# Kernel tuning notes

Hardware: AMD Instinct MI355X
Metric: run time of the kernel (lower is better)

The kernel has to match this reference:

```python
import jax, jax.numpy as jnp
import numpy as np

N_NODES = 100000
N_EDGES = 1600000
D_IN = 128
D_OUT = 128


def setup_inputs() -> dict:
    key = jax.random.key(0)
    k1, k2, k3, k4, k5 = jax.random.split(key, 5)
    x = jax.random.normal(k1, (N_NODES, D_IN), dtype=jnp.float32)
    # nn.Linear weight has shape [out_features, in_features]
    W = jax.random.normal(k2, (D_OUT, D_IN), dtype=jnp.float32) * (1.0 / np.sqrt(D_IN))
    adj_rows = jax.random.randint(k3, (N_EDGES,), 0, N_NODES, dtype=jnp.int32)
    adj_cols = jax.random.randint(k4, (N_EDGES,), 0, N_NODES, dtype=jnp.int32)
    adj_vals = jax.random.uniform(k5, (N_EDGES,), dtype=jnp.float32)
    return {"x": x, "W": W, "adj_rows": adj_rows, "adj_cols": adj_cols, "adj_vals": adj_vals}


def reference(x, W, adj_rows, adj_cols, adj_vals):
    # x: [N, D_in] node features; W: [D_out, D_in] linear weight (bias=False)
    h = jnp.einsum('ni,oi->no', x, W)  # dense projection, [N, D_out]
    # sparse adjacency matmul: out[r] = sum_e vals[e] * h[cols[e]] for rows[e]==r
    messages = adj_vals[:, None] * h[adj_cols]  # [E, D_out]
    out = jax.ops.segment_sum(messages, adj_rows, num_segments=x.shape[0])
    return out
```

## Files before the change

kernel.cpp:

```cpp
#include <hip/hip_runtime.h>

#define D 128
#define RPB 512
#define RPB_SHIFT 9
#define HALF 256
#define BUCKMAX 256
#define TILE 8192
#define SEGCAP 7168

typedef short bf16x8 __attribute__((ext_vector_type(8)));
typedef float f32x4 __attribute__((ext_vector_type(4)));

__device__ inline unsigned short f2bf(float f) {
    unsigned u = __float_as_uint(f);
    unsigned r = u + 0x7FFFu + ((u >> 16) & 1u);
    return (unsigned short)(r >> 16);
}

__global__ __launch_bounds__(256) void cast_bf16(const float* __restrict__ src,
                                                 unsigned short* __restrict__ dst,
                                                 long long n4) {
    long long i = (long long)blockIdx.x * 256 + threadIdx.x;
    const long long stride = (long long)gridDim.x * 256;
    for (; i < n4; i += stride) {
        float4 v = reinterpret_cast<const float4*>(src)[i];
        ushort4 o;
        o.x = f2bf(v.x); o.y = f2bf(v.y); o.z = f2bf(v.z); o.w = f2bf(v.w);
        reinterpret_cast<ushort4*>(dst)[i] = o;
    }
}

__global__ __launch_bounds__(1024) void bucket_hist(const int* __restrict__ rows,
                                                    int* __restrict__ bucketCnt,
                                                    int E, int NBUCK) {
    __shared__ int h[BUCKMAX];
    for (int i = threadIdx.x; i < NBUCK; i += 1024) h[i] = 0;
    __syncthreads();
    const int t0 = blockIdx.x * TILE;
    const int tend = min(t0 + TILE, E);
    for (int i = t0 + threadIdx.x; i < tend; i += 1024)
        atomicAdd(&h[rows[i] >> RPB_SHIFT], 1);
    __syncthreads();
    for (int i = threadIdx.x; i < NBUCK; i += 1024)
        if (h[i]) atomicAdd(&bucketCnt[i], h[i]);
}

__global__ __launch_bounds__(256) void bucket_scan(const int* __restrict__ bucketCnt,
                                                   int* __restrict__ bucketBase,
                                                   int* __restrict__ bucketCur,
                                                   int* __restrict__ offsets,
                                                   int NBUCK, int N) {
    __shared__ int t[256];
    const int tid = threadIdx.x;
    int v = (tid < NBUCK) ? bucketCnt[tid] : 0;
    t[tid] = v;
    __syncthreads();
    for (int ofs = 1; ofs < 256; ofs <<= 1) {
        int add = (tid >= ofs) ? t[tid - ofs] : 0;
        __syncthreads();
        t[tid] += add;
        __syncthreads();
    }
    if (tid < NBUCK) {
        bucketBase[tid] = t[tid] - v;
        bucketCur[tid] = 0;
    }
    if (tid == NBUCK - 1) {
        bucketBase[NBUCK] = t[tid];
        offsets[N] = t[tid];
    }
}

__global__ __launch_bounds__(1024) void binA(const int* __restrict__ rows,
                                             const int* __restrict__ cols,
                                             const float* __restrict__ vals,
                                             const int* __restrict__ bucketBase,
                                             int* __restrict__ bucketCur,
                                             uint2* __restrict__ pairs_bin,
                                             int E, int NBUCK) {
    __shared__ int h[BUCKMAX];
    __shared__ int base[BUCKMAX];
    const int t0 = blockIdx.x * TILE;
    const int tend = min(t0 + TILE, E);
    for (int i = threadIdx.x; i < NBUCK; i += 1024) h[i] = 0;
    __syncthreads();
    for (int i = t0 + threadIdx.x; i < tend; i += 1024)
        atomicAdd(&h[rows[i] >> RPB_SHIFT], 1);
    __syncthreads();
    for (int i = threadIdx.x; i < NBUCK; i += 1024) {
        int c = h[i];
        base[i] = c ? bucketBase[i] + atomicAdd(&bucketCur[i], c) : 0;
        h[i] = 0;
    }
    __syncthreads();
    for (int i = t0 + threadIdx.x; i < tend; i += 1024) {
        int r = rows[i];
        int b = r >> RPB_SHIFT;
        int p = base[b] + atomicAdd(&h[b], 1);
        unsigned pk = ((unsigned)(r & (RPB - 1)) << 23) | (unsigned)cols[i];
        pairs_bin[p] = make_uint2(pk, __float_as_uint(vals[i]));
    }
}

__global__ __launch_bounds__(256) void csr_build(const uint2* __restrict__ pairs_bin,
                                                 const int* __restrict__ bucketBase,
                                                 int* __restrict__ offsets,
                                                 uint2* __restrict__ pairs_g, int N) {
    __shared__ int hist[HALF];
    __shared__ int cur[HALF];
    __shared__ int tsum[256];
    __shared__ uint2 pr[SEGCAP];
    __shared__ int cntBelowSh;
    const int tid = threadIdx.x;
    const int buck = blockIdx.x >> 1, half = blockIdx.x & 1;
    const int lrow0 = half * HALF;
    const int grow0 = buck * RPB + lrow0;
    const int rbeg = bucketBase[buck], rend = bucketBase[buck + 1];

    hist[tid] = 0;
    if (tid == 0) cntBelowSh = 0;
    __syncthreads();

    int below = 0;
    for (int i = rbeg + tid; i < rend; i += 256) {
        int d = (int)(pairs_bin[i].x >> 23) - lrow0;
        if ((unsigned)d < (unsigned)HALF) atomicAdd(&hist[d], 1);
        else if (d < 0) ++below;
    }
    if (below) atomicAdd(&cntBelowSh, below);
    __syncthreads();

    int part = hist[tid];
    tsum[tid] = part;
    __syncthreads();
    for (int ofs = 1; ofs < 256; ofs <<= 1) {
        int add = (tid >= ofs) ? tsum[tid - ofs] : 0;
        __syncthreads();
        tsum[tid] += add;
        __syncthreads();
    }
    const int excl = tsum[tid] - part;
    const int segcnt = tsum[255];
    const int segbase = rbeg + cntBelowSh;

    cur[tid] = excl;
    const int grow = grow0 + tid;
    if (grow < N) offsets[grow] = segbase + excl;
    __syncthreads();

    if (segcnt <= SEGCAP) {
        for (int i = rbeg + tid; i < rend; i += 256) {
            uint2 e = pairs_bin[i];
            int d = (int)(e.x >> 23) - lrow0;
            if ((unsigned)d < (unsigned)HALF) {
                int p = atomicAdd(&cur[d], 1);
                pr[p] = make_uint2(e.x & 0x7FFFFFu, e.y);
            }
        }
        __syncthreads();
        for (int p = tid; p < segcnt; p += 256) pairs_g[segbase + p] = pr[p];
    } else {
        for (int i = rbeg + tid; i < rend; i += 256) {
            uint2 e = pairs_bin[i];
            int d = (int)(e.x >> 23) - lrow0;
            if ((unsigned)d < (unsigned)HALF) {
                int p = atomicAdd(&cur[d], 1);
                pairs_g[segbase + p] = make_uint2(e.x & 0x7FFFFFu, e.y);
            }
        }
    }
}

__global__ __launch_bounds__(256) void csr_gather_bf16(
    const unsigned short* __restrict__ xb,
    const int* __restrict__ offsets,
    const uint2* __restrict__ pairs,
    unsigned short* __restrict__ yb, int N) {
    const int row = blockIdx.x * 4 + (threadIdx.x >> 6);
    if (row >= N) return;
    const int lane = threadIdx.x & 63;
    const int beg = offsets[row], end = offsets[row + 1];
    float ax = 0.f, ay = 0.f;

    for (int base = beg; base < end; base += 64) {
        const int rem = min(end - base, 64);
        uint2 e = make_uint2(0u, 0u);
        if (lane < rem) e = pairs[base + lane];
        int c = (int)e.x;
        float v = __uint_as_float(e.y);

        for (int j0 = 0; j0 < rem; j0 += 8) {
            int cj[8];
            float vj[8];
            unsigned u[8];
#pragma unroll
            for (int jj = 0; jj < 8; ++jj) {
                cj[jj] = __shfl(c, j0 + jj);
                vj[jj] = __shfl(v, j0 + jj);
            }
#pragma unroll
            for (int jj = 0; jj < 8; ++jj)
                u[jj] = *reinterpret_cast<const unsigned*>(
                    xb + (size_t)cj[jj] * D + lane * 2);
#pragma unroll
            for (int jj = 0; jj < 8; ++jj) {
                ax = fmaf(vj[jj], __uint_as_float(u[jj] << 16), ax);
                ay = fmaf(vj[jj], __uint_as_float(u[jj] & 0xFFFF0000u), ay);
            }
        }
    }
    unsigned o = (unsigned)f2bf(ax) | ((unsigned)f2bf(ay) << 16);
    *reinterpret_cast<unsigned*>(yb + (size_t)row * D + lane * 2) = o;
}

__global__ __launch_bounds__(256) void gemm_mfma(const unsigned short* __restrict__ yb,
                                                 const unsigned short* __restrict__ Wb,
                                                 float* __restrict__ out, int N) {
    const int wid  = threadIdx.x >> 6;
    const int lane = threadIdx.x & 63;
    const int m0   = blockIdx.x * 64 + wid * 16;
    const int r    = lane & 15;
    const int kg   = lane >> 4;
    const int arow = m0 + r;

    f32x4 acc[8] = {};
#pragma unroll
    for (int ks = 0; ks < 4; ++ks) {
        const int k0 = ks * 32 + kg * 8;
        bf16x8 a = {};
        if (arow < N) a = *reinterpret_cast<const bf16x8*>(yb + (size_t)arow * D + k0);
#pragma unroll
        for (int t = 0; t < 8; ++t) {
            bf16x8 b = *reinterpret_cast<const bf16x8*>(Wb + (size_t)(t * 16 + r) * D + k0);
            acc[t] = __builtin_amdgcn_mfma_f32_16x16x32_bf16(a, b, acc[t], 0, 0, 0);
        }
    }
#pragma unroll
    for (int t = 0; t < 8; ++t) {
#pragma unroll
        for (int i = 0; i < 4; ++i) {
            const int row = m0 + kg * 4 + i;
            if (row < N) out[(size_t)row * D + t * 16 + r] = acc[t][i];
        }
    }
}

__global__ __launch_bounds__(256) void gemm64(const float* __restrict__ x,
                                              const float* __restrict__ W,
                                              float* __restrict__ h, int N) {
    __shared__ float xs[128][64];
    __shared__ float ws[128][64];
    const int tid = threadIdx.x;
    const int m0 = blockIdx.x * 64;
    const int n0 = blockIdx.y * 64;
    for (int idx = tid; idx < 2048; idx += 256) {
        int q = idx >> 6, m = idx & 63;
        int grow = m0 + m;
        float4 v = make_float4(0.f, 0.f, 0.f, 0.f);
        if (grow < N) v = *reinterpret_cast<const float4*>(x + (size_t)grow * D + q * 4);
        xs[q * 4 + 0][m] = v.x; xs[q * 4 + 1][m] = v.y;
        xs[q * 4 + 2][m] = v.z; xs[q * 4 + 3][m] = v.w;
    }
    for (int idx = tid; idx < 2048; idx += 256) {
        int q = idx >> 6, n = idx & 63;
        float4 v = *reinterpret_cast<const float4*>(W + (size_t)(n0 + n) * D + q * 4);
        ws[q * 4 + 0][n] = v.x; ws[q * 4 + 1][n] = v.y;
        ws[q * 4 + 2][n] = v.z; ws[q * 4 + 3][n] = v.w;
    }
    __syncthreads();
    const int tm = (tid & 15) * 4;
    const int tn = (tid >> 4) * 4;
    float acc[4][4] = {};
#pragma unroll 4
    for (int k = 0; k < 128; ++k) {
        float4 a4 = *reinterpret_cast<const float4*>(&xs[k][tm]);
        float4 b4 = *reinterpret_cast<const float4*>(&ws[k][tn]);
        float a[4] = {a4.x, a4.y, a4.z, a4.w};
        float b[4] = {b4.x, b4.y, b4.z, b4.w};
#pragma unroll
        for (int rr = 0; rr < 4; ++rr)
#pragma unroll
            for (int cc = 0; cc < 4; ++cc) acc[rr][cc] = fmaf(a[rr], b[cc], acc[rr][cc]);
    }
#pragma unroll
    for (int rr = 0; rr < 4; ++rr) {
        int row = m0 + tm + rr;
        if (row < N) {
            float4 o = make_float4(acc[rr][0], acc[rr][1], acc[rr][2], acc[rr][3]);
            *reinterpret_cast<float4*>(h + (size_t)row * D + n0 + tn) = o;
        }
    }
}

__global__ __launch_bounds__(256) void scatter_edges(const float* __restrict__ h,
                                                     const int* __restrict__ rows,
                                                     const int* __restrict__ cols,
                                                     const float* __restrict__ vals,
                                                     float* __restrict__ out, int E) {
    int t = blockIdx.x * 256 + threadIdx.x;
    int e = t >> 5;
    if (e >= E) return;
    int q = t & 31;
    int r = rows[e];
    int c = cols[e];
    float v = vals[e];
    float4 m = reinterpret_cast<const float4*>(h + (size_t)c * D)[q];
    float* op = out + (size_t)r * D + q * 4;
    atomicAdd(op + 0, v * m.x);
    atomicAdd(op + 1, v * m.y);
    atomicAdd(op + 2, v * m.z);
    atomicAdd(op + 3, v * m.w);
}

extern "C" void kernel_launch(void* const* d_in, const int* in_sizes, int n_in,
                              void* d_out, int out_size, void* d_ws, size_t ws_size,
                              hipStream_t stream) {
    const float* x        = (const float*)d_in[0];
    const float* W        = (const float*)d_in[1];
    const int*   adj_rows = (const int*)d_in[2];
    const int*   adj_cols = (const int*)d_in[3];
    const float* adj_vals = (const float*)d_in[4];
    float* out = (float*)d_out;

    const int N = in_sizes[0] / D;
    const int E = in_sizes[2];
    const int NBUCK = (N + RPB - 1) / RPB;
    const int NT = (E + TILE - 1) / TILE;

    size_t off = 0;
    auto carve = [&](size_t bytes) {
        void* p = (char*)d_ws + off;
        off += (bytes + 255) & ~(size_t)255;
        return p;
    };
    unsigned short* xb = (unsigned short*)carve((size_t)N * D * 2);
    unsigned short* yb = (unsigned short*)carve((size_t)N * D * 2);
    unsigned short* Wb = (unsigned short*)carve((size_t)D * D * 2);
    int* offsets    = (int*)carve((size_t)(N + 1) * sizeof(int));
    int* bucketCnt  = (int*)carve((size_t)BUCKMAX * sizeof(int));
    int* bucketBase = (int*)carve((size_t)(BUCKMAX + 1) * sizeof(int));
    int* bucketCur  = (int*)carve((size_t)BUCKMAX * sizeof(int));
    const size_t wsNeed = off;

    size_t doff = 0;
    auto carveOut = [&](size_t bytes) {
        void* p = (char*)d_out + doff;
        doff += (bytes + 255) & ~(size_t)255;
        return p;
    };
    uint2* pairs_bin = (uint2*)carveOut((size_t)E * sizeof(uint2));
    uint2* pairs_g   = (uint2*)carveOut((size_t)E * sizeof(uint2));
    const size_t doutNeed = doff;

    const bool fits = (wsNeed <= ws_size) &&
                      (doutNeed <= (size_t)out_size * sizeof(float)) &&
                      (NBUCK <= BUCKMAX) && (N < (1 << 23));

    if (fits) {
        cast_bf16<<<2048, 256, 0, stream>>>(x, xb, (long long)N * (D / 4));
        cast_bf16<<<16, 256, 0, stream>>>(W, Wb, (long long)D * (D / 4));
        hipMemsetAsync(bucketCnt, 0, (size_t)BUCKMAX * sizeof(int), stream);
        bucket_hist<<<NT, 1024, 0, stream>>>(adj_rows, bucketCnt, E, NBUCK);
        bucket_scan<<<1, 256, 0, stream>>>(bucketCnt, bucketBase, bucketCur,
                                           offsets, NBUCK, N);
        binA<<<NT, 1024, 0, stream>>>(adj_rows, adj_cols, adj_vals, bucketBase,
                                      bucketCur, pairs_bin, E, NBUCK);
        csr_build<<<NBUCK * 2, 256, 0, stream>>>(pairs_bin, bucketBase,
                                                 offsets, pairs_g, N);
        csr_gather_bf16<<<(N + 3) / 4, 256, 0, stream>>>(xb, offsets, pairs_g, yb, N);
        gemm_mfma<<<(N + 63) / 64, 256, 0, stream>>>(yb, Wb, out, N);
    } else {
        float* h = (float*)d_ws;
        hipMemsetAsync(d_out, 0, (size_t)out_size * sizeof(float), stream);
        dim3 ggrid((N + 63) / 64, D / 64);
        gemm64<<<ggrid, 256, 0, stream>>>(x, W, h, N);
        const long long tt = (long long)E * 32;
        scatter_edges<<<(int)((tt + 255) / 256), 256, 0, stream>>>(
            h, adj_rows, adj_cols, adj_vals, out, E);
    }
}
```

Measured before the change: 161.1 us.

## Fuse CSR gather with MFMA projection via LDS and merge setup kernels

Merges the gather and GEMM kernels so each 64-row block keeps its aggregated bf16 rows in swizzled LDS and applies the weight through MFMA directly. This removes the global round trip of the intermediate yb. The x cast is also fused with the bucket histogram, and the W cast with the bucket scan, cutting kernel launches. Gather unroll grows from 8 to 16, and the pair buffers move from the output buffer into workspace. The tradeoff is that each wave now processes 16 rows serially with fewer blocks, which reduces parallelism in the latency-bound gather.

```diff
diff --git a/kernel.cpp b/kernel.cpp
--- a/kernel.cpp
+++ b/kernel.cpp
@@ -17,41 +17,50 @@
     return (unsigned short)(r >> 16);
 }
 
-__global__ __launch_bounds__(256) void cast_bf16(const float* __restrict__ src,
-                                                 unsigned short* __restrict__ dst,
-                                                 long long n4) {
-    long long i = (long long)blockIdx.x * 256 + threadIdx.x;
-    const long long stride = (long long)gridDim.x * 256;
-    for (; i < n4; i += stride) {
-        float4 v = reinterpret_cast<const float4*>(src)[i];
+__global__ __launch_bounds__(256) void cast_x_hist(const float* __restrict__ x,
+                                                   unsigned short* __restrict__ xb,
+                                                   long long n4,
+                                                   const int* __restrict__ rows,
+                                                   int* __restrict__ bucketCnt,
+                                                   int E, int NBUCK) {
+    {
+        long long i = (long long)blockIdx.x * 256 + threadIdx.x;
+        const long long stride = (long long)gridDim.x * 256;
+        for (; i < n4; i += stride) {
+            float4 v = reinterpret_cast<const float4*>(x)[i];
+            ushort4 o;
+            o.x = f2bf(v.x); o.y = f2bf(v.y); o.z = f2bf(v.z); o.w = f2bf(v.w);
+            reinterpret_cast<ushort4*>(xb)[i] = o;
+        }
+    }
+    __shared__ int h[BUCKMAX];
+    for (int i = threadIdx.x; i < BUCKMAX; i += 256) h[i] = 0;
+    __syncthreads();
+    {
+        long long i = (long long)blockIdx.x * 256 + threadIdx.x;
+        const long long stride = (long long)gridDim.x * 256;
+        for (; i < E; i += stride) atomicAdd(&h[rows[i] >> RPB_SHIFT], 1);
+    }
+    __syncthreads();
+    for (int i = threadIdx.x; i < NBUCK; i += 256)
+        if (h[i]) atomicAdd(&bucketCnt[i], h[i]);
+}
+
+__global__ __launch_bounds__(256) void scan_castW(const float* __restrict__ W,
+                                                  unsigned short* __restrict__ Wb,
+                                                  const int* __restrict__ bucketCnt,
+                                                  int* __restrict__ bucketBase,
+                                                  int* __restrict__ bucketCur,
+                                                  int* __restrict__ offsets,
+                                                  int NBUCK, int N) {
+    const int tid = threadIdx.x;
+    for (int idx = tid; idx < D * D / 4; idx += 256) {
+        float4 v = reinterpret_cast<const float4*>(W)[idx];
         ushort4 o;
         o.x = f2bf(v.x); o.y = f2bf(v.y); o.z = f2bf(v.z); o.w = f2bf(v.w);
-        reinterpret_cast<ushort4*>(dst)[i] = o;
-    }
-}
-
-__global__ __launch_bounds__(1024) void bucket_hist(const int* __restrict__ rows,
-                                                    int* __restrict__ bucketCnt,
-                                                    int E, int NBUCK) {
-    __shared__ int h[BUCKMAX];
-    for (int i = threadIdx.x; i < NBUCK; i += 1024) h[i] = 0;
-    __syncthreads();
-    const int t0 = blockIdx.x * TILE;
-    const int tend = min(t0 + TILE, E);
-    for (int i = t0 + threadIdx.x; i < tend; i += 1024)
-        atomicAdd(&h[rows[i] >> RPB_SHIFT], 1);
-    __syncthreads();
-    for (int i = threadIdx.x; i < NBUCK; i += 1024)
-        if (h[i]) atomicAdd(&bucketCnt[i], h[i]);
-}
-
-__global__ __launch_bounds__(256) void bucket_scan(const int* __restrict__ bucketCnt,
-                                                   int* __restrict__ bucketBase,
-                                                   int* __restrict__ bucketCur,
-                                                   int* __restrict__ offsets,
-                                                   int NBUCK, int N) {
+        reinterpret_cast<ushort4*>(Wb)[idx] = o;
+    }
     __shared__ int t[256];
-    const int tid = threadIdx.x;
     int v = (tid < NBUCK) ? bucketCnt[tid] : 0;
     t[tid] = v;
     __syncthreads();
@@ -171,64 +180,68 @@
     }
 }
 
-__global__ __launch_bounds__(256) void csr_gather_bf16(
+__global__ __launch_bounds__(256) void spmm_fused(
     const unsigned short* __restrict__ xb,
     const int* __restrict__ offsets,
     const uint2* __restrict__ pairs,
-    unsigned short* __restrict__ yb, int N) {
-    const int row = blockIdx.x * 4 + (threadIdx.x >> 6);
-    if (row >= N) return;
+    const unsigned short* __restrict__ Wb,
+    float* __restrict__ out, int N) {
+    __shared__ unsigned short ylds[64 * D];
+    const int wid = threadIdx.x >> 6;
     const int lane = threadIdx.x & 63;
-    const int beg = offsets[row], end = offsets[row + 1];
-    float ax = 0.f, ay = 0.f;
-
-    for (int base = beg; base < end; base += 64) {
-        const int rem = min(end - base, 64);
-        uint2 e = make_uint2(0u, 0u);
-        if (lane < rem) e = pairs[base + lane];
-        int c = (int)e.x;
-        float v = __uint_as_float(e.y);
-
-        for (int j0 = 0; j0 < rem; j0 += 8) {
-            int cj[8];
-            float vj[8];
-            unsigned u[8];
-#pragma unroll
-            for (int jj = 0; jj < 8; ++jj) {
-                cj[jj] = __shfl(c, j0 + jj);
-                vj[jj] = __shfl(v, j0 + jj);
+    const int row0 = blockIdx.x * 64;
+
+    for (int rr = 0; rr < 16; ++rr) {
+        const int lr = wid * 16 + rr;
+        const int grow = row0 + lr;
+        float ax = 0.f, ay = 0.f;
+        if (grow < N) {
+            const int beg = offsets[grow], end = offsets[grow + 1];
+            for (int base = beg; base < end; base += 64) {
+                const int rem = min(end - base, 64);
+                uint2 e = make_uint2(0u, 0u);
+                if (lane < rem) e = pairs[base + lane];
+                int c = (int)e.x;
+                float v = __uint_as_float(e.y);
+
+                for (int j0 = 0; j0 < rem; j0 += 16) {
+                    int cj[16];
+                    float vj[16];
+                    unsigned u[16];
+#pragma unroll
+                    for (int jj = 0; jj < 16; ++jj) {
+                        cj[jj] = __shfl(c, j0 + jj);
+                        vj[jj] = __shfl(v, j0 + jj);
+                    }
+#pragma unroll
+                    for (int jj = 0; jj < 16; ++jj)
+                        u[jj] = *reinterpret_cast<const unsigned*>(
+                            xb + (size_t)cj[jj] * D + lane * 2);
+#pragma unroll
+                    for (int jj = 0; jj < 16; ++jj) {
+                        ax = fmaf(vj[jj], __uint_as_float(u[jj] << 16), ax);
+                        ay = fmaf(vj[jj], __uint_as_float(u[jj] & 0xFFFF0000u), ay);
+                    }
+                }
             }
-#pragma unroll
-            for (int jj = 0; jj < 8; ++jj)
-                u[jj] = *reinterpret_cast<const unsigned*>(
-                    xb + (size_t)cj[jj] * D + lane * 2);
-#pragma unroll
-            for (int jj = 0; jj < 8; ++jj) {
-                ax = fmaf(vj[jj], __uint_as_float(u[jj] << 16), ax);
-                ay = fmaf(vj[jj], __uint_as_float(u[jj] & 0xFFFF0000u), ay);
-            }
-        }
-    }
-    unsigned o = (unsigned)f2bf(ax) | ((unsigned)f2bf(ay) << 16);
-    *reinterpret_cast<unsigned*>(yb + (size_t)row * D + lane * 2) = o;
-}
-
-__global__ __launch_bounds__(256) void gemm_mfma(const unsigned short* __restrict__ yb,
-                                                 const unsigned short* __restrict__ Wb,
-                                                 float* __restrict__ out, int N) {
-    const int wid  = threadIdx.x >> 6;
-    const int lane = threadIdx.x & 63;
-    const int m0   = blockIdx.x * 64 + wid * 16;
-    const int r    = lane & 15;
-    const int kg   = lane >> 4;
-    const int arow = m0 + r;
+        }
+        const unsigned o = (unsigned)f2bf(ax) | ((unsigned)f2bf(ay) << 16);
+        const int byteoff = lr * 256 + ((lane * 4) ^ ((lr & 7) << 4));
+        *reinterpret_cast<unsigned*>(reinterpret_cast<char*>(ylds) + byteoff) = o;
+    }
+    __syncthreads();
+
+    const int r = lane & 15;
+    const int kg = lane >> 4;
+    const int lr_a = wid * 16 + r;
 
     f32x4 acc[8] = {};
 #pragma unroll
     for (int ks = 0; ks < 4; ++ks) {
         const int k0 = ks * 32 + kg * 8;
-        bf16x8 a = {};
-        if (arow < N) a = *reinterpret_cast<const bf16x8*>(yb + (size_t)arow * D + k0);
+        const int abyte = lr_a * 256 + ((k0 * 2) ^ ((lr_a & 7) << 4));
+        bf16x8 a = *reinterpret_cast<const bf16x8*>(
+            reinterpret_cast<const char*>(ylds) + abyte);
 #pragma unroll
         for (int t = 0; t < 8; ++t) {
             bf16x8 b = *reinterpret_cast<const bf16x8*>(Wb + (size_t)(t * 16 + r) * D + k0);
@@ -239,7 +252,7 @@
     for (int t = 0; t < 8; ++t) {
 #pragma unroll
         for (int i = 0; i < 4; ++i) {
-            const int row = m0 + kg * 4 + i;
+            const int row = row0 + wid * 16 + kg * 4 + i;
             if (row < N) out[(size_t)row * D + t * 16 + r] = acc[t][i];
         }
     }
@@ -334,41 +347,29 @@
         return p;
     };
     unsigned short* xb = (unsigned short*)carve((size_t)N * D * 2);
-    unsigned short* yb = (unsigned short*)carve((size_t)N * D * 2);
     unsigned short* Wb = (unsigned short*)carve((size_t)D * D * 2);
     int* offsets    = (int*)carve((size_t)(N + 1) * sizeof(int));
     int* bucketCnt  = (int*)carve((size_t)BUCKMAX * sizeof(int));
     int* bucketBase = (int*)carve((size_t)(BUCKMAX + 1) * sizeof(int));
     int* bucketCur  = (int*)carve((size_t)BUCKMAX * sizeof(int));
+    uint2* pairs_bin = (uint2*)carve((size_t)E * sizeof(uint2));
+    uint2* pairs_g   = (uint2*)carve((size_t)E * sizeof(uint2));
     const size_t wsNeed = off;
 
-    size_t doff = 0;
-    auto carveOut = [&](size_t bytes) {
-        void* p = (char*)d_out + doff;
-        doff += (bytes + 255) & ~(size_t)255;
-        return p;
-    };
-    uint2* pairs_bin = (uint2*)carveOut((size_t)E * sizeof(uint2));
-    uint2* pairs_g   = (uint2*)carveOut((size_t)E * sizeof(uint2));
-    const size_t doutNeed = doff;
-
-    const bool fits = (wsNeed <= ws_size) &&
-                      (doutNeed <= (size_t)out_size * sizeof(float)) &&
-                      (NBUCK <= BUCKMAX) && (N < (1 << 23));
+    const bool fits = (wsNeed <= ws_size) && (NBUCK <= BUCKMAX) && (N < (1 << 23));
 
     if (fits) {
-        cast_bf16<<<2048, 256, 0, stream>>>(x, xb, (long long)N * (D / 4));
-        cast_bf16<<<16, 256, 0, stream>>>(W, Wb, (long long)D * (D / 4));
         hipMemsetAsync(bucketCnt, 0, (size_t)BUCKMAX * sizeof(int), stream);
-        bucket_hist<<<NT, 1024, 0, stream>>>(adj_rows, bucketCnt, E, NBUCK);
-        bucket_scan<<<1, 256, 0, stream>>>(bucketCnt, bucketBase, bucketCur,
-                                           offsets, NBUCK, N);
+        cast_x_hist<<<2048, 256, 0, stream>>>(x, xb, (long long)N * (D / 4),
+                                              adj_rows, bucketCnt, E, NBUCK);
+        scan_castW<<<1, 256, 0, stream>>>(W, Wb, bucketCnt, bucketBase, bucketCur,
+                                          offsets, NBUCK, N);
         binA<<<NT, 1024, 0, stream>>>(adj_rows, adj_cols, adj_vals, bucketBase,
                                       bucketCur, pairs_bin, E, NBUCK);
         csr_build<<<NBUCK * 2, 256, 0, stream>>>(pairs_bin, bucketBase,
                                                  offsets, pairs_g, N);
-        csr_gather_bf16<<<(N + 3) / 4, 256, 0, stream>>>(xb, offsets, pairs_g, yb, N);
-        gemm_mfma<<<(N + 63) / 64, 256, 0, stream>>>(yb, Wb, out, N);
+        spmm_fused<<<(N + 63) / 64, 256, 0, stream>>>(xb, offsets, pairs_g, Wb,
+                                                      out, N);
     } else {
         float* h = (float*)d_ws;
         hipMemsetAsync(d_out, 0, (size_t)out_size * sizeof(float), stream);
```

Measured after the change: 201.0 us. 24.8% more time.
